# Optimization experiments

Hardware: AMD Instinct MI355X
Metric: run time of the kernel (lower is better)

Reference implementation:

```python
import jax, jax.numpy as jnp
import numpy as np

DECAY = 0.9


def setup_inputs() -> dict:
    key = jax.random.key(0)
    ks = jax.random.split(key, 8)
    B, L, d_model = 4, 2048, 1024
    d_state = 16
    d_inner = 2 * d_model  # expand=2
    x = jax.random.normal(ks[0], (B, L, d_model), dtype=jnp.float32)
    Win = jax.random.normal(ks[1], (d_model, d_inner), dtype=jnp.float32) / np.sqrt(d_model)
    bin_ = jnp.zeros((d_inner,), dtype=jnp.float32)
    Bp = jax.random.normal(ks[2], (d_inner, d_state), dtype=jnp.float32) * 0.01
    Cp = jax.random.normal(ks[3], (d_state, d_inner), dtype=jnp.float32) * 0.01
    Dp = jnp.ones((d_inner,), dtype=jnp.float32)
    Wout = jax.random.normal(ks[4], (d_inner, d_model), dtype=jnp.float32) / np.sqrt(d_inner)
    bout = jnp.zeros((d_model,), dtype=jnp.float32)
    return {"x": x, "Win": Win, "bin_": bin_, "Bp": Bp, "Cp": Cp, "Dp": Dp,
            "Wout": Wout, "bout": bout}


def reference(x, Win, bin_, Bp, Cp, Dp, Wout, bout):
    # x: [B, L, d_model]
    B, L, _ = x.shape
    d_inner, d_state = Bp.shape
    xi = jax.nn.silu(x @ Win + bin_)          # [B, L, d_inner]
    xt_seq = jnp.swapaxes(xi, 0, 1)            # [L, B, d_inner] for scan over time

    def step(h, xt):
        # h: [B, d_inner, d_state]; xt: [B, d_inner]
        h = h * DECAY + xt[:, :, None] * Bp[None, :, :]
        y = jnp.einsum('bij,ji->bi', h, Cp) + Dp * xt
        return h, y

    h0 = jnp.zeros((B, d_inner, d_state), dtype=x.dtype)
    _, ys = jax.lax.scan(step, h0, xt_seq)     # ys: [L, B, d_inner]
    y = jnp.swapaxes(ys, 0, 1)                 # [B, L, d_inner]
    return y @ Wout + bout                     # [B, L, d_model]
```

## Files before the change

### kernel.cpp

```cpp
#include <hip/hip_runtime.h>
#include <hip/hip_bf16.h>
#include <cstdint>
#include <cstddef>

typedef __attribute__((ext_vector_type(8))) short short8_t;
typedef __attribute__((ext_vector_type(4))) float f32x4;

__device__ __forceinline__ void gload16(const void* g, void* l) {
  __builtin_amdgcn_global_load_lds(
      (const __attribute__((address_space(1))) void*)g,
      (__attribute__((address_space(3))) void*)l, 16, 0, 0);
}

#define BARRIER() do { asm volatile("" ::: "memory"); __builtin_amdgcn_s_barrier(); asm volatile("" ::: "memory"); } while (0)
#define LGKM0 asm volatile("s_waitcnt lgkmcnt(0)" ::: "memory")
#define WVM(n) asm volatile("s_waitcnt vmcnt(" #n ")" ::: "memory")

__global__ __launch_bounds__(256) void cvt_bf16_kernel(
    const float* __restrict__ in, __hip_bfloat16* __restrict__ out, int n) {
  int gid = blockIdx.x * blockDim.x + threadIdx.x;
  int idx = gid * 4;
  if (idx >= n) return;
  float4 v = *reinterpret_cast<const float4*>(in + idx);
  union { short4 s4; __hip_bfloat16 h[4]; } u;
  u.h[0] = __float2bfloat16(v.x);
  u.h[1] = __float2bfloat16(v.y);
  u.h[2] = __float2bfloat16(v.z);
  u.h[3] = __float2bfloat16(v.w);
  *reinterpret_cast<short4*>(out + idx) = u.s4;
}

__global__ __launch_bounds__(256) void transpose_cvt_kernel(
    const float* __restrict__ in, __hip_bfloat16* __restrict__ out, int R, int C) {
  __shared__ float tile[32][33];
  int c0 = blockIdx.x * 32, r0 = blockIdx.y * 32;
  int tx = threadIdx.x, ty = threadIdx.y;
#pragma unroll
  for (int j = 0; j < 32; j += 8)
    tile[ty + j][tx] = in[(size_t)(r0 + ty + j) * C + c0 + tx];
  __syncthreads();
#pragma unroll
  for (int j = 0; j < 32; j += 8)
    out[(size_t)(c0 + ty + j) * R + r0 + tx] = __float2bfloat16(tile[tx][ty + j]);
}

template <int EPI>
__global__ __launch_bounds__(512, 2) void gemm_seg_kernel(
    const __hip_bfloat16* __restrict__ A,
    const __hip_bfloat16* __restrict__ Bt,
    const float* __restrict__ bias,
    void* __restrict__ Cout,
    int M, int N, int K) {
  constexpr int AUNIT = 32768, BUNIT = 16384;
  constexpr int BOFF = 3 * AUNIT;
  __shared__ int4 ldsv[(3 * AUNIT + 3 * BUNIT) / 16];
  char* lds = (char*)ldsv;

  const int tid = threadIdx.x;
  const int l = tid & 63;
  const int w = tid >> 6;
  const int wm = w >> 1, wn = w & 1;
  const int fr = l & 15;
  const int q16 = (l >> 4) * 16;
  const int swz = (fr & 7) << 4;
  const int arow_base = (wm * 64 + fr) * 128;
  const int brow_base = (wn * 64 + fr) * 128;

  const int nbn = N / 128;
  int bid = blockIdx.x;
  const int cpx = gridDim.x >> 3;
  bid = (bid & 7) * cpx + (bid >> 3);
  const int brow = (bid / nbn) * 256;
  const int bcol = (bid % nbn) * 128;
  const size_t K2 = (size_t)K * 2;

  int srow[4], scol[4], dstw[4];
#pragma unroll
  for (int j = 0; j < 4; ++j) {
    int d = j * 8192 + tid * 16;
    int lg = d ^ (((d >> 7) & 7) << 4);
    srow[j] = lg >> 7;  scol[j] = lg & 127;
    dstw[j] = j * 8192 + w * 1024;
  }

  const char* Abp = (const char*)A;
  const char* Bbp = (const char*)Bt;

  auto stT = [&](int t, int ab) {
#pragma unroll
    for (int j = 0; j < 4; ++j)
      gload16(Abp + (size_t)(brow + srow[j]) * K2 + (size_t)t * 128 + scol[j],
              lds + ab + dstw[j]);
#pragma unroll
    for (int j = 0; j < 2; ++j)
      gload16(Bbp + (size_t)(bcol + srow[j]) * K2 + (size_t)t * 128 + scol[j],
              lds + BOFF + ab / 2 + dstw[j]);
  };

  f32x4 acc[4][4];
#pragma unroll
  for (int m = 0; m < 4; ++m)
#pragma unroll
    for (int n = 0; n < 4; ++n) acc[m][n] = (f32x4)0.f;

  const int NT = K >> 6;
  stT(0, 0); stT(1, AUNIT);
  WVM(6); BARRIER();

  int curA = 0, stAb = 2 * AUNIT;
  for (int T = 0; T < NT; ++T) {
    short8_t af[8], bf[8];
#pragma unroll
    for (int kh = 0; kh < 2; ++kh) {
      const int ko = (kh * 64 + q16) ^ swz;
#pragma unroll
      for (int mi = 0; mi < 4; ++mi)
        af[kh * 4 + mi] = *(const short8_t*)(lds + curA + arow_base + mi * 2048 + ko);
#pragma unroll
      for (int n = 0; n < 4; ++n)
        bf[kh * 4 + n] = *(const short8_t*)(lds + BOFF + curA / 2 + brow_base + n * 2048 + ko);
    }
    if (T + 2 < NT) stT(T + 2, stAb);
#pragma unroll
    for (int kh = 0; kh < 2; ++kh)
#pragma unroll
      for (int mi = 0; mi < 4; ++mi)
#pragma unroll
        for (int n = 0; n < 4; ++n)
          acc[mi][n] = __builtin_amdgcn_mfma_f32_16x16x32_bf16(
              af[kh * 4 + mi], bf[kh * 4 + n], acc[mi][n], 0, 0, 0);
    if (T + 1 < NT) {
      if (T + 2 < NT) { WVM(6); } else { WVM(0); }
      LGKM0;
      BARRIER();
    }
    curA += AUNIT; if (curA == 3 * AUNIT) curA = 0;
    stAb += AUNIT; if (stAb == 3 * AUNIT) stAb = 0;
  }

  const int r0 = brow + wm * 64 + (l >> 4) * 4;
  const int c0 = bcol + wn * 64 + fr;
#pragma unroll
  for (int m = 0; m < 4; ++m) {
#pragma unroll
    for (int n = 0; n < 4; ++n) {
      const int col = c0 + n * 16;
      const float bv = bias[col];
#pragma unroll
      for (int j = 0; j < 4; ++j) {
        const int row = r0 + m * 16 + j;
        float v = acc[m][n][j] + bv;
        if constexpr (EPI == 0) {
          v = v / (1.0f + __expf(-v));
          ((__hip_bfloat16*)Cout)[(size_t)row * N + col] = __float2bfloat16(v);
        } else {
          ((float*)Cout)[(size_t)row * N + col] = v;
        }
      }
    }
  }
}

__global__ __launch_bounds__(256) void scan_kernel(
    const __hip_bfloat16* __restrict__ xi,
    const float* __restrict__ Bp,
    const float* __restrict__ Cp,
    const float* __restrict__ Dp,
    __hip_bfloat16* __restrict__ y) {
  constexpr int L = 2048, DI = 2048, DS = 16, TW = 256, H = 32;
  const int tid = threadIdx.x;
  const int bidx = blockIdx.x;
  const int iblk = bidx & 7;
  const int chunk = (bidx >> 3) & 7;
  const int b = bidx >> 6;
  const int i = iblk * 256 + tid;

  float cb = 0.f;
#pragma unroll
  for (int s = 0; s < DS; ++s) cb += Bp[i * DS + s] * Cp[s * DI + i];
  const float dp = Dp[i];

  const int t0 = chunk * TW;
  int tstart = t0 - H;
  if (tstart < 0) tstart = 0;

  const __hip_bfloat16* xp = xi + (size_t)(b * L) * DI + i;
  __hip_bfloat16* yp = y + (size_t)(b * L) * DI + i;

  float g = 0.f;
  const __hip_bfloat16* p = xp + (size_t)tstart * DI;
  for (int t = tstart; t < t0; ++t, p += DI)
    g = g * 0.9f + __bfloat162float(*p);
  __hip_bfloat16* q = yp + (size_t)t0 * DI;
  for (int t = 0; t < TW; ++t, p += DI, q += DI) {
    float xv = __bfloat162float(*p);
    g = g * 0.9f + xv;
    *q = __float2bfloat16(cb * g + dp * xv);
  }
}

extern "C" void kernel_launch(void* const* d_in, const int* in_sizes, int n_in,
                              void* d_out, int out_size, void* d_ws, size_t ws_size,
                              hipStream_t stream) {
  const float* x    = (const float*)d_in[0];
  const float* Win  = (const float*)d_in[1];
  const float* bin  = (const float*)d_in[2];
  const float* Bp   = (const float*)d_in[3];
  const float* Cp   = (const float*)d_in[4];
  const float* Dp   = (const float*)d_in[5];
  const float* Wout = (const float*)d_in[6];
  const float* bout = (const float*)d_in[7];
  float* out = (float*)d_out;

  constexpr int Bb = 4, L = 2048, DM = 1024, DI = 2048;
  constexpr int Mrows = Bb * L;

  char* ws = (char*)d_ws;
  __hip_bfloat16* xb    = (__hip_bfloat16*)ws;
  __hip_bfloat16* WinT  = (__hip_bfloat16*)(ws + (16u << 20));
  __hip_bfloat16* WoutT = (__hip_bfloat16*)(ws + (20u << 20));
  __hip_bfloat16* xi    = (__hip_bfloat16*)(ws + (24u << 20));
  __hip_bfloat16* yb    = (__hip_bfloat16*)(ws + (56u << 20));

  {
    int n = Mrows * DM;
    cvt_bf16_kernel<<<n / 1024, 256, 0, stream>>>(x, xb, n);
  }
  transpose_cvt_kernel<<<dim3(DI / 32, DM / 32), dim3(32, 8), 0, stream>>>(Win, WinT, DM, DI);
  transpose_cvt_kernel<<<dim3(DM / 32, DI / 32), dim3(32, 8), 0, stream>>>(Wout, WoutT, DI, DM);
  gemm_seg_kernel<0><<<(Mrows / 256) * (DI / 128), 512, 0, stream>>>(
      xb, WinT, bin, (void*)xi, Mrows, DI, DM);
  scan_kernel<<<Bb * (L / 256) * (DI / 256), 256, 0, stream>>>(xi, Bp, Cp, Dp, yb);
  gemm_seg_kernel<1><<<(Mrows / 256) * (DM / 128), 512, 0, stream>>>(
      yb, WoutT, bout, (void*)out, Mrows, DM, DI);
}
```

Measured before the change: 129.0 us.

## Merge preprocessing kernels and switch GEMM to 128x128 tiles with 5-stage pipeline

The three conversion and transpose kernels become one launch that dispatches on block index, which saves launch overhead. The GEMM moves from 256x128 tiles with a 3-buffer ring to 128x128 tiles with a 5-buffer LDS ring, prefetching four K-steps ahead. The warp layout changes to 2x4, and occupancy is lowered to 1 block per CU because the kernel now uses about 160KB of LDS. Smaller tiles double the grid size and deepen latency hiding, at the cost of more B/A reloads and less MFMA work per LDS read.

Result: slower. 146.4 us (+13.5%).

```diff
diff --git a/kernel.cpp b/kernel.cpp
--- a/kernel.cpp
+++ b/kernel.cpp
@@ -16,25 +16,30 @@
 #define LGKM0 asm volatile("s_waitcnt lgkmcnt(0)" ::: "memory")
 #define WVM(n) asm volatile("s_waitcnt vmcnt(" #n ")" ::: "memory")
 
-__global__ __launch_bounds__(256) void cvt_bf16_kernel(
-    const float* __restrict__ in, __hip_bfloat16* __restrict__ out, int n) {
-  int gid = blockIdx.x * blockDim.x + threadIdx.x;
-  int idx = gid * 4;
-  if (idx >= n) return;
-  float4 v = *reinterpret_cast<const float4*>(in + idx);
-  union { short4 s4; __hip_bfloat16 h[4]; } u;
-  u.h[0] = __float2bfloat16(v.x);
-  u.h[1] = __float2bfloat16(v.y);
-  u.h[2] = __float2bfloat16(v.z);
-  u.h[3] = __float2bfloat16(v.w);
-  *reinterpret_cast<short4*>(out + idx) = u.s4;
-}
-
-__global__ __launch_bounds__(256) void transpose_cvt_kernel(
-    const float* __restrict__ in, __hip_bfloat16* __restrict__ out, int R, int C) {
+__global__ __launch_bounds__(256) void preproc_kernel(
+    const float* __restrict__ x, __hip_bfloat16* __restrict__ xb,
+    const float* __restrict__ Win, __hip_bfloat16* __restrict__ WinT,
+    const float* __restrict__ Wout, __hip_bfloat16* __restrict__ WoutT) {
   __shared__ float tile[32][33];
-  int c0 = blockIdx.x * 32, r0 = blockIdx.y * 32;
-  int tx = threadIdx.x, ty = threadIdx.y;
+  const int b = blockIdx.x;
+  const int tid = threadIdx.x;
+  if (b < 8192) {
+    int idx = (b * 256 + tid) * 4;
+    float4 v = *reinterpret_cast<const float4*>(x + idx);
+    union { short4 s4; __hip_bfloat16 h[4]; } u;
+    u.h[0] = __float2bfloat16(v.x);
+    u.h[1] = __float2bfloat16(v.y);
+    u.h[2] = __float2bfloat16(v.z);
+    u.h[3] = __float2bfloat16(v.w);
+    *reinterpret_cast<short4*>(xb + idx) = u.s4;
+    return;
+  }
+  const float* in;  __hip_bfloat16* out;  int R, C, tb;
+  if (b < 8192 + 2048) { tb = b - 8192;  in = Win;  out = WinT;  R = 1024; C = 2048; }
+  else                 { tb = b - 10240; in = Wout; out = WoutT; R = 2048; C = 1024; }
+  const int nbx = C / 32;
+  const int c0 = (tb % nbx) * 32, r0 = (tb / nbx) * 32;
+  const int tx = tid & 31, ty = tid >> 5;
 #pragma unroll
   for (int j = 0; j < 32; j += 8)
     tile[ty + j][tx] = in[(size_t)(r0 + ty + j) * C + c0 + tx];
@@ -45,38 +50,38 @@
 }
 
 template <int EPI>
-__global__ __launch_bounds__(512, 2) void gemm_seg_kernel(
+__global__ __launch_bounds__(512, 1) void gemm5r_kernel(
     const __hip_bfloat16* __restrict__ A,
     const __hip_bfloat16* __restrict__ Bt,
     const float* __restrict__ bias,
     void* __restrict__ Cout,
     int M, int N, int K) {
-  constexpr int AUNIT = 32768, BUNIT = 16384;
-  constexpr int BOFF = 3 * AUNIT;
-  __shared__ int4 ldsv[(3 * AUNIT + 3 * BUNIT) / 16];
+  constexpr int UNIT = 16384;
+  constexpr int BOFF = 5 * UNIT;
+  __shared__ int4 ldsv[(10 * UNIT) / 16];
   char* lds = (char*)ldsv;
 
   const int tid = threadIdx.x;
   const int l = tid & 63;
   const int w = tid >> 6;
-  const int wm = w >> 1, wn = w & 1;
+  const int wm = w >> 2, wn = w & 3;
   const int fr = l & 15;
   const int q16 = (l >> 4) * 16;
   const int swz = (fr & 7) << 4;
   const int arow_base = (wm * 64 + fr) * 128;
-  const int brow_base = (wn * 64 + fr) * 128;
+  const int brow_base = (wn * 32 + fr) * 128;
 
   const int nbn = N / 128;
   int bid = blockIdx.x;
   const int cpx = gridDim.x >> 3;
   bid = (bid & 7) * cpx + (bid >> 3);
-  const int brow = (bid / nbn) * 256;
+  const int brow = (bid / nbn) * 128;
   const int bcol = (bid % nbn) * 128;
   const size_t K2 = (size_t)K * 2;
 
-  int srow[4], scol[4], dstw[4];
-#pragma unroll
-  for (int j = 0; j < 4; ++j) {
+  int srow[2], scol[2], dstw[2];
+#pragma unroll
+  for (int j = 0; j < 2; ++j) {
     int d = j * 8192 + tid * 16;
     int lg = d ^ (((d >> 7) & 7) << 4);
     srow[j] = lg >> 7;  scol[j] = lg & 127;
@@ -86,64 +91,67 @@
   const char* Abp = (const char*)A;
   const char* Bbp = (const char*)Bt;
 
-  auto stT = [&](int t, int ab) {
-#pragma unroll
-    for (int j = 0; j < 4; ++j)
+  auto stT = [&](int t, int buf) {
+#pragma unroll
+    for (int j = 0; j < 2; ++j)
       gload16(Abp + (size_t)(brow + srow[j]) * K2 + (size_t)t * 128 + scol[j],
-              lds + ab + dstw[j]);
+              lds + buf * UNIT + dstw[j]);
 #pragma unroll
     for (int j = 0; j < 2; ++j)
       gload16(Bbp + (size_t)(bcol + srow[j]) * K2 + (size_t)t * 128 + scol[j],
-              lds + BOFF + ab / 2 + dstw[j]);
+              lds + BOFF + buf * UNIT + dstw[j]);
   };
 
-  f32x4 acc[4][4];
+  f32x4 acc[4][2];
 #pragma unroll
   for (int m = 0; m < 4; ++m)
 #pragma unroll
-    for (int n = 0; n < 4; ++n) acc[m][n] = (f32x4)0.f;
+    for (int n = 0; n < 2; ++n) acc[m][n] = (f32x4)0.f;
 
   const int NT = K >> 6;
-  stT(0, 0); stT(1, AUNIT);
-  WVM(6); BARRIER();
-
-  int curA = 0, stAb = 2 * AUNIT;
+  stT(0, 0); stT(1, 1); stT(2, 2); stT(3, 3);
+  WVM(12); BARRIER();
+
+  int cur = 0, bst = 4;
   for (int T = 0; T < NT; ++T) {
-    short8_t af[8], bf[8];
+    if (T + 4 < NT) stT(T + 4, bst);
+    short8_t af[8], bf[4];
 #pragma unroll
     for (int kh = 0; kh < 2; ++kh) {
       const int ko = (kh * 64 + q16) ^ swz;
 #pragma unroll
       for (int mi = 0; mi < 4; ++mi)
-        af[kh * 4 + mi] = *(const short8_t*)(lds + curA + arow_base + mi * 2048 + ko);
-#pragma unroll
-      for (int n = 0; n < 4; ++n)
-        bf[kh * 4 + n] = *(const short8_t*)(lds + BOFF + curA / 2 + brow_base + n * 2048 + ko);
+        af[kh * 4 + mi] = *(const short8_t*)(lds + cur * UNIT + arow_base + mi * 2048 + ko);
+#pragma unroll
+      for (int n = 0; n < 2; ++n)
+        bf[kh * 2 + n] = *(const short8_t*)(lds + BOFF + cur * UNIT + brow_base + n * 2048 + ko);
     }
-    if (T + 2 < NT) stT(T + 2, stAb);
 #pragma unroll
     for (int kh = 0; kh < 2; ++kh)
 #pragma unroll
       for (int mi = 0; mi < 4; ++mi)
 #pragma unroll
-        for (int n = 0; n < 4; ++n)
+        for (int n = 0; n < 2; ++n)
           acc[mi][n] = __builtin_amdgcn_mfma_f32_16x16x32_bf16(
-              af[kh * 4 + mi], bf[kh * 4 + n], acc[mi][n], 0, 0, 0);
+              af[kh * 4 + mi], bf[kh * 2 + n], acc[mi][n], 0, 0, 0);
     if (T + 1 < NT) {
-      if (T + 2 < NT) { WVM(6); } else { WVM(0); }
+      if (T + 4 < NT)      { WVM(12); }
+      else if (T + 3 < NT) { WVM(8); }
+      else if (T + 2 < NT) { WVM(4); }
+      else                 { WVM(0); }
       LGKM0;
       BARRIER();
     }
-    curA += AUNIT; if (curA == 3 * AUNIT) curA = 0;
-    stAb += AUNIT; if (stAb == 3 * AUNIT) stAb = 0;
+    cur = (cur == 4) ? 0 : cur + 1;
+    bst = (bst == 4) ? 0 : bst + 1;
   }
 
   const int r0 = brow + wm * 64 + (l >> 4) * 4;
-  const int c0 = bcol + wn * 64 + fr;
+  const int c0 = bcol + wn * 32 + fr;
 #pragma unroll
   for (int m = 0; m < 4; ++m) {
 #pragma unroll
-    for (int n = 0; n < 4; ++n) {
+    for (int n = 0; n < 2; ++n) {
       const int col = c0 + n * 16;
       const float bv = bias[col];
 #pragma unroll
@@ -222,15 +230,11 @@
   __hip_bfloat16* xi    = (__hip_bfloat16*)(ws + (24u << 20));
   __hip_bfloat16* yb    = (__hip_bfloat16*)(ws + (56u << 20));
 
-  {
-    int n = Mrows * DM;
-    cvt_bf16_kernel<<<n / 1024, 256, 0, stream>>>(x, xb, n);
-  }
-  transpose_cvt_kernel<<<dim3(DI / 32, DM / 32), dim3(32, 8), 0, stream>>>(Win, WinT, DM, DI);
-  transpose_cvt_kernel<<<dim3(DM / 32, DI / 32), dim3(32, 8), 0, stream>>>(Wout, WoutT, DI, DM);
-  gemm_seg_kernel<0><<<(Mrows / 256) * (DI / 128), 512, 0, stream>>>(
+  preproc_kernel<<<8192 + 2048 + 2048, 256, 0, stream>>>(
+      x, xb, Win, WinT, Wout, WoutT);
+  gemm5r_kernel<0><<<(Mrows / 128) * (DI / 128), 512, 0, stream>>>(
       xb, WinT, bin, (void*)xi, Mrows, DI, DM);
   scan_kernel<<<Bb * (L / 256) * (DI / 256), 256, 0, stream>>>(xi, Bp, Cp, Dp, yb);
-  gemm_seg_kernel<1><<<(Mrows / 256) * (DM / 128), 512, 0, stream>>>(
+  gemm5r_kernel<1><<<(Mrows / 128) * (DM / 128), 512, 0, stream>>>(
       yb, WoutT, bout, (void*)out, Mrows, DM, DI);
 }
```
